# Optimization experiments

Hardware: AMD Instinct MI355X
Metric: run time of the kernel (lower is better)

Reference implementation:

```python
import jax, jax.numpy as jnp
import numpy as np

EPS = 1e-3  # keras BatchNormalization default epsilon
NUM_HEADS = 8


def conv1d_same(x, w, b):
    # x: [B,T,Cin], w: [K,Cin,Cout]
    return jax.lax.conv_general_dilated(
        x, w, window_strides=(1,), padding='SAME',
        dimension_numbers=('NWC', 'WIO', 'NWC')) + b


def bn(x, g, b, m, v):
    # inference-mode batchnorm with moving stats
    return (x - m) * jax.lax.rsqrt(v + EPS) * g + b


def lstm(x, K, R, b):
    # x: [B,T,D] -> [B,T,U]; keras gate order i,f,c,o; recurrent_dropout off at inference
    B = x.shape[0]
    U = R.shape[0]
    xp = jnp.einsum('btd,dz->btz', x, K) + b  # precompute input projection

    def step(carry, xt):
        h, c = carry
        z = xt + h @ R
        i, f, g, o = jnp.split(z, 4, axis=-1)
        c = jax.nn.sigmoid(f) * c + jax.nn.sigmoid(i) * jnp.tanh(g)
        h = jax.nn.sigmoid(o) * jnp.tanh(c)
        return (h, c), h

    h0 = jnp.zeros((B, U), x.dtype)
    _, hs = jax.lax.scan(step, (h0, h0), jnp.swapaxes(xp, 0, 1))
    return jnp.swapaxes(hs, 0, 1)


def bilstm(x, Kf, Rf, bf, Kb, Rb, bb):
    fwd = lstm(x, Kf, Rf, bf)
    bwd = lstm(x[:, ::-1], Kb, Rb, bb)[:, ::-1]
    return jnp.concatenate([fwd, bwd], axis=-1)


def mhsa(x, wq, bq, wk, bk, wv, bv, wo, bo):
    B, T, _ = x.shape
    d_model = wq.shape[1]
    dh = d_model // NUM_HEADS
    q = (x @ wq + bq).reshape(B, T, NUM_HEADS, dh)
    k = (x @ wk + bk).reshape(B, T, NUM_HEADS, dh)
    v = (x @ wv + bv).reshape(B, T, NUM_HEADS, dh)
    logits = jnp.einsum('bqhd,bkhd->bhqk', q, k) / jnp.sqrt(jnp.asarray(dh, x.dtype))
    attn = jax.nn.softmax(logits, axis=-1)
    out = jnp.einsum('bhqk,bkhd->bqhd', attn, v).reshape(B, T, d_model)
    return out @ wo + bo


def setup_inputs() -> dict:
    key = jax.random.key(0)
    ks = iter(jax.random.split(key, 64))

    def nrm(shape, s=0.05):
        return (jax.random.normal(next(ks), shape) * s).astype(jnp.float32)

    p = {}
    p['x'] = jax.random.normal(next(ks), (512, 256, 78), dtype=jnp.float32)
    for name, shp in [
            ('conv5_w', (5, 78, 64)), ('conv7_w', (7, 78, 64)), ('conv9_w', (9, 78, 64)),
            ('fuse_w', (1, 192, 128)), ('se_w1', (128, 8)), ('se_w2', (8, 128)),
            ('l1f_k', (128, 512)), ('l1f_r', (128, 512)), ('l1b_k', (128, 512)), ('l1b_r', (128, 512)),
            ('l2f_k', (256, 256)), ('l2f_r', (64, 256)), ('l2b_k', (256, 256)), ('l2b_r', (64, 256)),
            ('wq', (128, 256)), ('wk', (128, 256)), ('wv', (128, 256)), ('wo', (256, 256)),
            ('d1_w', (256, 256)), ('d2_w', (256, 128)), ('d3_w', (128, 1)),
            ('conv5_b', (64,)), ('conv7_b', (64,)), ('conv9_b', (64,)), ('fuse_b', (128,)),
            ('se_b1', (8,)), ('se_b2', (128,)),
            ('l1f_b', (512,)), ('l1b_b', (512,)), ('l2f_b', (256,)), ('l2b_b', (256,)),
            ('bq', (256,)), ('bk', (256,)), ('bv', (256,)), ('bo', (256,)),
            ('d1_b', (256,)), ('d2_b', (128,)), ('d3_b', (1,))]:
        p[name] = nrm(shp)
    for tag, c in [('bn5', 64), ('bn7', 64), ('bn9', 64), ('bn_l1', 256),
                   ('bn_l2', 128), ('bn_d1', 256), ('bn_d2', 128)]:
        p[tag + '_g'] = jnp.ones((c,), jnp.float32)
        p[tag + '_b'] = jnp.zeros((c,), jnp.float32)
        p[tag + '_m'] = jnp.zeros((c,), jnp.float32)
        p[tag + '_v'] = jnp.ones((c,), jnp.float32)
    return p


def reference(x, conv5_w, conv5_b, bn5_g, bn5_b, bn5_m, bn5_v,
              conv7_w, conv7_b, bn7_g, bn7_b, bn7_m, bn7_v,
              conv9_w, conv9_b, bn9_g, bn9_b, bn9_m, bn9_v,
              fuse_w, fuse_b, se_w1, se_b1, se_w2, se_b2,
              l1f_k, l1f_r, l1f_b, l1b_k, l1b_r, l1b_b,
              bn_l1_g, bn_l1_b, bn_l1_m, bn_l1_v,
              l2f_k, l2f_r, l2f_b, l2b_k, l2b_r, l2b_b,
              bn_l2_g, bn_l2_b, bn_l2_m, bn_l2_v,
              wq, bq, wk, bk, wv, bv, wo, bo,
              d1_w, d1_b, bn_d1_g, bn_d1_b, bn_d1_m, bn_d1_v,
              d2_w, d2_b, bn_d2_g, bn_d2_b, bn_d2_m, bn_d2_v,
              d3_w, d3_b):
    def block(w, b, g, bt, m, v):
        h = jax.nn.relu(conv1d_same(x, w, b))
        h = bn(h, g, bt, m, v)
        B, T, C = h.shape  # MaxPooling1D(2, 'same'); T is even
        return h.reshape(B, T // 2, 2, C).max(axis=2)

    fused = jnp.concatenate([
        block(conv5_w, conv5_b, bn5_g, bn5_b, bn5_m, bn5_v),
        block(conv7_w, conv7_b, bn7_g, bn7_b, bn7_m, bn7_v),
        block(conv9_w, conv9_b, bn9_g, bn9_b, bn9_m, bn9_v)], axis=-1)
    fused = conv1d_same(fused, fuse_w, fuse_b)

    # SENet spatial attention
    s = fused.mean(axis=1)
    e = jax.nn.sigmoid(jax.nn.relu(s @ se_w1 + se_b1) @ se_w2 + se_b2)
    h = fused * e[:, None, :]

    h = bilstm(h, l1f_k, l1f_r, l1f_b, l1b_k, l1b_r, l1b_b)
    h = bn(h, bn_l1_g, bn_l1_b, bn_l1_m, bn_l1_v)
    h = bilstm(h, l2f_k, l2f_r, l2f_b, l2b_k, l2b_r, l2b_b)
    h = bn(h, bn_l2_g, bn_l2_b, bn_l2_m, bn_l2_v)

    h = mhsa(h, wq, bq, wk, bk, wv, bv, wo, bo)
    g_ = h.mean(axis=1)

    d = jax.nn.relu(g_ @ d1_w + d1_b)
    d = bn(d, bn_d1_g, bn_d1_b, bn_d1_m, bn_d1_v)
    d = jax.nn.relu(d @ d2_w + d2_b)
    d = bn(d, bn_d2_g, bn_d2_b, bn_d2_m, bn_d2_v)
    return jax.nn.sigmoid(d @ d3_w + d3_b)
```

## Files before the change

### kernel.cpp

```cpp
#include <hip/hip_runtime.h>

#define EPS 1e-3f

typedef __attribute__((ext_vector_type(8))) short bf16x8;
typedef __attribute__((ext_vector_type(4))) float f32x4;

__device__ __forceinline__ float sigm(float x){ return 1.0f/(1.0f + __expf(-x)); }
__device__ __forceinline__ float tanhfast(float x){ return 1.0f - 2.0f/(1.0f + __expf(2.0f*x)); }

__device__ __forceinline__ unsigned short f2b(float f){
    union { float f; unsigned u; } v; v.f = f;
    unsigned r = v.u + 0x7FFFu + ((v.u >> 16) & 1u);
    return (unsigned short)(r >> 16);
}
__device__ __forceinline__ float b2f(unsigned short h){
    union { unsigned u; float f; } v; v.u = ((unsigned)h) << 16; return v.f;
}

__global__ void __launch_bounds__(256)
prep_x(const float* __restrict__ x, unsigned short* __restrict__ xbf)
{
    const int b = blockIdx.x;
    const float* xs = x + (size_t)b*256*78;
    unsigned short* xd = xbf + (size_t)b*264*96;
    for (int p = threadIdx.x; p < 264*48; p += 256){
        int row = p / 48;
        int cp  = (p - row*48) * 2;
        int t   = row - 4;
        unsigned short v0 = 0, v1 = 0;
        if (t >= 0 && t < 256){
            if (cp   < 78) v0 = f2b(xs[t*78 + cp]);
            if (cp+1 < 78) v1 = f2b(xs[t*78 + cp + 1]);
        }
        *(unsigned int*)(xd + row*96 + cp) = (unsigned)v0 | ((unsigned)v1 << 16);
    }
}

__global__ void __launch_bounds__(256)
prep_w(const float* __restrict__ w5, const float* __restrict__ w7, const float* __restrict__ w9,
       unsigned short* __restrict__ wfrag)
{
    int g = blockIdx.x*256 + threadIdx.x;
    if (g >= 27*12*64) return;
    union { unsigned short s[8]; uint4 v; } u;
    int base = g * 8;
    #pragma unroll
    for (int e = 0; e < 8; ++e){
        int lin  = base + e;
        int slot = lin & 511;
        int fi   = lin >> 9;
        int nt   = fi % 12, kcs = fi / 12;
        int k    = kcs / 3, cs = kcs - k*3;
        int l15  = slot >> 5, r = slot & 31;
        int lg   = r >> 3, ee = r & 7;
        int ci   = cs*32 + lg*8 + ee;
        int co   = nt*16 + l15;
        float val = 0.f;
        if (ci < 78){
            if (co < 64){
                int kk = k - 2;
                if (kk >= 0 && kk < 5) val = w5[(kk*78 + ci)*64 + co];
            } else if (co < 128){
                int kk = k - 1;
                if (kk >= 0 && kk < 7) val = w7[(kk*78 + ci)*64 + (co - 64)];
            } else {
                val = w9[(k*78 + ci)*64 + (co - 128)];
            }
        }
        u.s[e] = f2b(val);
    }
    *(uint4*)(wfrag + base) = u.v;
}

__global__ void prep_ss(const float* b5, const float* b7, const float* b9,
                        const float* g5, const float* be5, const float* m5, const float* v5,
                        const float* g7, const float* be7, const float* m7, const float* v7,
                        const float* g9, const float* be9, const float* m9, const float* v9,
                        float* __restrict__ biascat, float* __restrict__ scale, float* __restrict__ shift)
{
    int c = threadIdx.x;
    if (c >= 192) return;
    float bv, g, be, m, v;
    if (c < 64){        bv=b5[c];      g=g5[c];      be=be5[c];      m=m5[c];      v=v5[c]; }
    else if (c < 128){  int i=c-64;  bv=b7[i]; g=g7[i]; be=be7[i]; m=m7[i]; v=v7[i]; }
    else {              int i=c-128; bv=b9[i]; g=g9[i]; be=be9[i]; m=m9[i]; v=v9[i]; }
    float s = g * rsqrtf(v + EPS);
    biascat[c] = bv;
    scale[c]   = s;
    shift[c]   = be - m*s;
}

__global__ void __launch_bounds__(256)
conv_mfma(const unsigned short* __restrict__ xbf,
          const unsigned short* __restrict__ wfrag,
          const float* __restrict__ biascat, const float* __restrict__ scale,
          const float* __restrict__ shift,
          float* __restrict__ out)
{
    const int b = blockIdx.x, tile = blockIdx.y;
    const int tid = threadIdx.x, lane = tid & 63, wv = tid >> 6;
    const int l15 = lane & 15, lg = lane >> 4;
    const int nt0 = wv * 3;
    const int t0  = tile * 64;

    f32x4 acc[4][3];
    #pragma unroll
    for (int nt = 0; nt < 3; ++nt){
        float bv = biascat[(nt0 + nt)*16 + l15];
        #pragma unroll
        for (int mt = 0; mt < 4; ++mt)
            acc[mt][nt] = (f32x4){bv, bv, bv, bv};
    }

    const unsigned short* xb = xbf + ((size_t)b*264 + t0 + l15)*96 + lg*8;
    const unsigned short* wb = wfrag + (size_t)nt0*512 + l15*32 + lg*8;

    for (int k = 0; k < 9; ++k){
        #pragma unroll
        for (int cs = 0; cs < 3; ++cs){
            bf16x8 A[4], Bf[3];
            #pragma unroll
            for (int mt = 0; mt < 4; ++mt)
                A[mt] = *(const bf16x8*)(xb + (size_t)(k + mt*16)*96 + cs*32);
            #pragma unroll
            for (int nt = 0; nt < 3; ++nt)
                Bf[nt] = *(const bf16x8*)(wb + (size_t)((k*3 + cs)*12 + nt)*512);
            #pragma unroll
            for (int mt = 0; mt < 4; ++mt)
                #pragma unroll
                for (int nt = 0; nt < 3; ++nt)
                    acc[mt][nt] = __builtin_amdgcn_mfma_f32_16x16x32_bf16(A[mt], Bf[nt], acc[mt][nt], 0, 0, 0);
        }
    }

    #pragma unroll
    for (int nt = 0; nt < 3; ++nt){
        int col = (nt0 + nt)*16 + l15;
        float s = scale[col], sh = shift[col];
        #pragma unroll
        for (int mt = 0; mt < 4; ++mt){
            float v0 = fmaxf(acc[mt][nt][0], 0.f)*s + sh;
            float v1 = fmaxf(acc[mt][nt][1], 0.f)*s + sh;
            float v2 = fmaxf(acc[mt][nt][2], 0.f)*s + sh;
            float v3 = fmaxf(acc[mt][nt][3], 0.f)*s + sh;
            int tb = tile*32 + mt*8 + lg*2;
            out[((size_t)b*128 + tb    )*192 + col] = fmaxf(v0, v1);
            out[((size_t)b*128 + tb + 1)*192 + col] = fmaxf(v2, v3);
        }
    }
}

__global__ void __launch_bounds__(256)
fuse_v2(const float* __restrict__ in,
        const float* __restrict__ w,
        const float* __restrict__ bias,
        float* __restrict__ out)
{
    __shared__ float xl[16][192];
    const int tid = threadIdx.x;
    const size_t row0 = (size_t)blockIdx.x * 16;

    {
        const float4* ip = (const float4*)(in + row0*192);
        float4* xp = (float4*)&xl[0][0];
        #pragma unroll
        for (int idx = tid; idx < 768; idx += 256) xp[idx] = ip[idx];
    }
    __syncthreads();

    const int co = tid & 127;
    const int rg = tid >> 7;
    float acc[8];
    {
        float bv = bias[co];
        #pragma unroll
        for (int r = 0; r < 8; ++r) acc[r] = bv;
    }

    for (int ci4 = 0; ci4 < 192; ci4 += 4){
        float wv0 = w[(ci4+0)*128 + co];
        float wv1 = w[(ci4+1)*128 + co];
        float wv2 = w[(ci4+2)*128 + co];
        float wv3 = w[(ci4+3)*128 + co];
        #pragma unroll
        for (int r = 0; r < 8; ++r){
            const float4 xr = *(const float4*)&xl[rg*8 + r][ci4];
            acc[r] = fmaf(xr.x, wv0, acc[r]);
            acc[r] = fmaf(xr.y, wv1, acc[r]);
            acc[r] = fmaf(xr.z, wv2, acc[r]);
            acc[r] = fmaf(xr.w, wv3, acc[r]);
        }
    }
    #pragma unroll
    for (int r = 0; r < 8; ++r)
        out[(row0 + rg*8 + r)*128 + co] = acc[r];
}

__global__ void se_kernel(float* __restrict__ fused,
                          const float* __restrict__ w1, const float* __restrict__ b1,
                          const float* __restrict__ w2, const float* __restrict__ b2)
{
    int b = blockIdx.x, c = threadIdx.x;
    __shared__ float sv[128];
    __shared__ float rv[8];
    float* fp = fused + (size_t)b*128*128 + c;
    float acc = 0.f;
    for (int t = 0; t < 128; ++t) acc += fp[t*128];
    sv[c] = acc * (1.f/128.f);
    __syncthreads();
    if (c < 8){
        float r = b1[c];
        for (int i = 0; i < 128; ++i) r = fmaf(sv[i], w1[i*8 + c], r);
        rv[c] = fmaxf(r, 0.f);
    }
    __syncthreads();
    float e = b2[c];
    #pragma unroll
    for (int j = 0; j < 8; ++j) e = fmaf(rv[j], w2[j*128 + c], e);
    e = sigm(e);
    for (int t = 0; t < 128; ++t) fp[t*128] *= e;
}

template<int K, bool ABF16, int OUTMODE>
__global__ void __launch_bounds__(256)
xp_gemm(const void* __restrict__ Av, const float* __restrict__ W,
        const float* __restrict__ bias, unsigned short* __restrict__ outp, int N)
{
    __shared__ unsigned short Asm[128][40];
    __shared__ unsigned short Bsm[8][64][8];

    const int tid  = threadIdx.x;
    const int lane = tid & 63;
    const int wv   = tid >> 6;
    const int wm   = wv & 1;
    const int wn   = wv >> 1;
    const size_t m0 = (size_t)blockIdx.x * 128;
    const int n0   = blockIdx.y * 128;

    f32x4 acc[4][4];
    #pragma unroll
    for (int nt = 0; nt < 4; ++nt){
        float bv = bias[n0 + wn*64 + nt*16 + (lane & 15)];
        #pragma unroll
        for (int mt = 0; mt < 4; ++mt)
            acc[mt][nt] = (f32x4){bv, bv, bv, bv};
    }

    const int bn = tid & 127;
    const int bg = tid >> 7;

    for (int k0 = 0; k0 < K; k0 += 32){
        __syncthreads();
        if constexpr (!ABF16){
            const float* Ag = (const float*)Av;
            #pragma unroll
            for (int i = 0; i < 2; ++i){
                int g = tid + i*256;
                int r = g >> 2, c8 = g & 3;
                float4 d0 = *(const float4*)(Ag + (m0 + r)*K + k0 + c8*8);
                float4 d1 = *(const float4*)(Ag + (m0 + r)*K + k0 + c8*8 + 4);
                union { unsigned short s[8]; uint4 v; } u;
                u.s[0]=f2b(d0.x); u.s[1]=f2b(d0.y); u.s[2]=f2b(d0.z); u.s[3]=f2b(d0.w);
                u.s[4]=f2b(d1.x); u.s[5]=f2b(d1.y); u.s[6]=f2b(d1.z); u.s[7]=f2b(d1.w);
                *(uint4*)&Asm[r][c8*8] = u.v;
            }
        } else {
            const unsigned short* Ag = (const unsigned short*)Av;
            #pragma unroll
            for (int i = 0; i < 2; ++i){
                int g = tid + i*256;
                int r = g >> 2, c8 = g & 3;
                uint4 d = *(const uint4*)(Ag + (m0 + r)*K + k0 + c8*8);
                *(uint4*)&Asm[r][c8*8] = d;
            }
        }
        {
            union { unsigned short s[8]; uint4 v; } u0, u1;
            #pragma unroll
            for (int q = 0; q < 8; ++q){
                u0.s[q] = f2b(W[(size_t)(k0 + bg*16 + q)*N + n0 + bn]);
                u1.s[q] = f2b(W[(size_t)(k0 + bg*16 + 8 + q)*N + n0 + bn]);
            }
            int nt = bn >> 4, lo = bn & 15;
            *(uint4*)&Bsm[nt][lo + 16*(2*bg)][0]   = u0.v;
            *(uint4*)&Bsm[nt][lo + 16*(2*bg+1)][0] = u1.v;
        }
        __syncthreads();

        bf16x8 af[4], bfr[4];
        #pragma unroll
        for (int mt = 0; mt < 4; ++mt)
            af[mt] = *(const bf16x8*)&Asm[wm*64 + mt*16 + (lane & 15)][(lane >> 4)*8];
        #pragma unroll
        for (int nt = 0; nt < 4; ++nt)
            bfr[nt] = *(const bf16x8*)&Bsm[wn*4 + nt][lane][0];
        #pragma unroll
        for (int mt = 0; mt < 4; ++mt)
            #pragma unroll
            for (int nt = 0; nt < 4; ++nt)
                acc[mt][nt] = __builtin_amdgcn_mfma_f32_16x16x32_bf16(af[mt], bfr[nt], acc[mt][nt], 0, 0, 0);
    }

    #pragma unroll
    for (int mt = 0; mt < 4; ++mt)
        #pragma unroll
        for (int nt = 0; nt < 4; ++nt)
            #pragma unroll
            for (int r = 0; r < 4; ++r){
                size_t row = m0 + wm*64 + mt*16 + (lane >> 4)*4 + r;
                int    col = n0 + wn*64 + nt*16 + (lane & 15);
                if constexpr (OUTMODE == 0){
                    outp[row*N + col] = f2b(acc[mt][nt][r]);
                } else {
                    size_t off = ((size_t)((row >> 7)*8 + (col >> 5))*32 + (col & 31))*128 + (row & 127);
                    outp[off] = f2b(acc[mt][nt][r]);
                }
            }
}

template<int U, bool OUT_BF16>
__global__ void __launch_bounds__(512)
lstm_rec(const unsigned short* __restrict__ xpf, const unsigned short* __restrict__ xpb,
         const float* __restrict__ Rf, const float* __restrict__ Rb,
         const float* __restrict__ bng, const float* __restrict__ bnb,
         const float* __restrict__ bnm, const float* __restrict__ bnv,
         void* __restrict__ outv, int dir_param)
{
    constexpr int Z   = 4*U;
    constexpr int KT  = U/32;
    constexpr int NTW = Z/128;
    constexpr int HP  = U + 8;

    __shared__ unsigned short h_lds[16][HP];
    __shared__ float z_lds[4][Z];

    const int tid  = threadIdx.x;
    const int lane = tid & 63;
    const int wv   = tid >> 6;
    const int dir  = (gridDim.y == 2) ? (int)blockIdx.y : dir_param;
    const int b0   = blockIdx.x * 4;
    const int ncol0 = wv * (Z/8);

    const unsigned short* xp = dir ? xpb : xpf;
    const float* Rg = dir ? Rb : Rf;

    for (int i = tid; i < 16*HP; i += 512) ((unsigned short*)h_lds)[i] = 0;

    bf16x8 rf[KT][NTW];
    {
        const int kb = (lane >> 4) * 8;
        const int nc = lane & 15;
        #pragma unroll
        for (int kt = 0; kt < KT; ++kt)
            #pragma unroll
            for (int nt = 0; nt < NTW; ++nt){
                union { unsigned short s[8]; bf16x8 v; } u;
                #pragma unroll
                for (int e = 0; e < 8; ++e)
                    u.s[e] = f2b(Rg[(size_t)(kt*32 + kb + e)*Z + ncol0 + nt*16 + nc]);
                rf[kt][nt] = u.v;
            }
    }

    const int u_  = tid % U;
    const int r_  = tid / U;
    const bool gate = (tid < 4*U);
    float c_ = 0.f;
    float bns = 0.f, bnsh = 0.f;
    const int ch = dir*U + u_;
    if (gate){
        bns  = bng[ch] * rsqrtf(bnv[ch] + EPS);
        bnsh = bnb[ch] - bnm[ch]*bns;
    }
    __syncthreads();

    for (int ts = 0; ts < 128; ++ts){
        const int t = dir ? 127 - ts : ts;
        unsigned short xq0=0,xq1=0,xq2=0,xq3=0;
        if (gate){
            const unsigned short* xr = xp + ((size_t)(b0 + r_)*128 + t)*Z + u_;
            xq0 = xr[0]; xq1 = xr[U]; xq2 = xr[2*U]; xq3 = xr[3*U];
        }
        bf16x8 af[KT];
        #pragma unroll
        for (int kt = 0; kt < KT; ++kt)
            af[kt] = *(const bf16x8*)&h_lds[lane & 15][kt*32 + (lane >> 4)*8];
        f32x4 acc[NTW];
        #pragma unroll
        for (int nt = 0; nt < NTW; ++nt) acc[nt] = (f32x4){0.f,0.f,0.f,0.f};
        #pragma unroll
        for (int kt = 0; kt < KT; ++kt)
            #pragma unroll
            for (int nt = 0; nt < NTW; ++nt)
                acc[nt] = __builtin_amdgcn_mfma_f32_16x16x32_bf16(af[kt], rf[kt][nt], acc[nt], 0, 0, 0);
        if ((lane >> 4) == 0){
            #pragma unroll
            for (int nt = 0; nt < NTW; ++nt)
                #pragma unroll
                for (int r = 0; r < 4; ++r)
                    z_lds[r][ncol0 + nt*16 + (lane & 15)] = acc[nt][r];
        }
        __syncthreads();
        if (gate){
            float z0 = z_lds[r_][u_      ] + b2f(xq0);
            float z1 = z_lds[r_][u_ +  U ] + b2f(xq1);
            float z2 = z_lds[r_][u_ + 2*U] + b2f(xq2);
            float z3 = z_lds[r_][u_ + 3*U] + b2f(xq3);
            float iv = sigm(z0), fv = sigm(z1), gv = tanhfast(z2), ov = sigm(z3);
            c_ = fv*c_ + iv*gv;
            float h = ov * tanhfast(c_);
            h_lds[r_][u_] = f2b(h);
            float hb = fmaf(h, bns, bnsh);
            size_t oidx = ((size_t)(b0 + r_)*128 + t)*(size_t)(2*U) + ch;
            if constexpr (OUT_BF16) ((unsigned short*)outv)[oidx] = f2b(hb);
            else                    ((float*)outv)[oidx] = hb;
        }
        __syncthreads();
    }
}

__global__ void __launch_bounds__(256)
attn_kernel(const unsigned short* __restrict__ qb,
            const unsigned short* __restrict__ kb,
            const unsigned short* __restrict__ vb,
            float* __restrict__ msum)
{
    __shared__ unsigned short p_lds[128][136];
    __shared__ float red[4][2][16];

    const int b  = blockIdx.x, hd = blockIdx.y;
    const int tid = threadIdx.x, lane = tid & 63, wv = tid >> 6;
    const int m0 = wv * 32;
    const int l15 = lane & 15, lg = lane >> 4;

    bf16x8 aq[2];
    #pragma unroll
    for (int mt = 0; mt < 2; ++mt)
        aq[mt] = *(const bf16x8*)(qb + ((size_t)(b*128 + m0 + mt*16 + l15))*256 + hd*32 + lg*8);

    bf16x8 bk[8];
    #pragma unroll
    for (int nt = 0; nt < 8; ++nt)
        bk[nt] = *(const bf16x8*)(kb + ((size_t)(b*128 + nt*16 + l15))*256 + hd*32 + lg*8);

    f32x4 s[2][8];
    #pragma unroll
    for (int mt = 0; mt < 2; ++mt)
        #pragma unroll
        for (int nt = 0; nt < 8; ++nt) s[mt][nt] = (f32x4){0.f,0.f,0.f,0.f};
    #pragma unroll
    for (int mt = 0; mt < 2; ++mt)
        #pragma unroll
        for (int nt = 0; nt < 8; ++nt)
            s[mt][nt] = __builtin_amdgcn_mfma_f32_16x16x32_bf16(aq[mt], bk[nt], s[mt][nt], 0, 0, 0);

    const float scale = 0.17677669529663687f;
    #pragma unroll
    for (int mt = 0; mt < 2; ++mt)
        #pragma unroll
        for (int r = 0; r < 4; ++r){
            float mx = -1e30f;
            #pragma unroll
            for (int nt = 0; nt < 8; ++nt) mx = fmaxf(mx, s[mt][nt][r]);
            #pragma unroll
            for (int msk = 1; msk < 16; msk <<= 1) mx = fmaxf(mx, __shfl_xor(mx, msk, 64));
            float pv[8], sum = 0.f;
            #pragma unroll
            for (int nt = 0; nt < 8; ++nt){
                pv[nt] = __expf((s[mt][nt][r] - mx) * scale);
                sum += pv[nt];
            }
            #pragma unroll
            for (int msk = 1; msk < 16; msk <<= 1) sum += __shfl_xor(sum, msk, 64);
            float inv = 1.f / sum;
            int row = m0 + mt*16 + lg*4 + r;
            #pragma unroll
            for (int nt = 0; nt < 8; ++nt)
                p_lds[row][nt*16 + l15] = f2b(pv[nt] * inv);
        }
    __syncthreads();

    f32x4 o[2][2];
    #pragma unroll
    for (int mt = 0; mt < 2; ++mt)
        #pragma unroll
        for (int dn = 0; dn < 2; ++dn) o[mt][dn] = (f32x4){0.f,0.f,0.f,0.f};
    bf16x8 bv[4][2];
    #pragma unroll
    for (int kt = 0; kt < 4; ++kt)
        #pragma unroll
        for (int dn = 0; dn < 2; ++dn)
            bv[kt][dn] = *(const bf16x8*)(vb + ((size_t)(b*8 + hd)*32 + dn*16 + l15)*128 + kt*32 + lg*8);
    #pragma unroll
    for (int mt = 0; mt < 2; ++mt)
        #pragma unroll
        for (int kt = 0; kt < 4; ++kt){
            bf16x8 ap = *(const bf16x8*)&p_lds[m0 + mt*16 + l15][kt*32 + lg*8];
            #pragma unroll
            for (int dn = 0; dn < 2; ++dn)
                o[mt][dn] = __builtin_amdgcn_mfma_f32_16x16x32_bf16(ap, bv[kt][dn], o[mt][dn], 0, 0, 0);
        }

    float sm[2];
    #pragma unroll
    for (int dn = 0; dn < 2; ++dn){
        float a = 0.f;
        #pragma unroll
        for (int mt = 0; mt < 2; ++mt)
            #pragma unroll
            for (int r = 0; r < 4; ++r) a += o[mt][dn][r];
        a += __shfl_xor(a, 16, 64);
        a += __shfl_xor(a, 32, 64);
        sm[dn] = a;
    }
    if (lg == 0){
        red[wv][0][l15] = sm[0];
        red[wv][1][l15] = sm[1];
    }
    __syncthreads();
    if (tid < 32){
        int dn = tid >> 4, n = tid & 15;
        float tot = red[0][dn][n] + red[1][dn][n] + red[2][dn][n] + red[3][dn][n];
        msum[(size_t)b*256 + hd*32 + dn*16 + n] = tot * (1.f/128.f);
    }
}

__global__ void __launch_bounds__(256)
head_kernel(const float* __restrict__ msum,
            const float* __restrict__ wo, const float* __restrict__ bo,
            const float* __restrict__ d1w, const float* __restrict__ d1b,
            const float* __restrict__ g1, const float* __restrict__ b1,
            const float* __restrict__ m1, const float* __restrict__ v1,
            const float* __restrict__ d2w, const float* __restrict__ d2b,
            const float* __restrict__ g2, const float* __restrict__ b2,
            const float* __restrict__ m2, const float* __restrict__ v2,
            const float* __restrict__ d3w, const float* __restrict__ d3b,
            float* __restrict__ outp)
{
    int b = blockIdx.x, j = threadIdx.x;
    __shared__ float s1[256];
    __shared__ float s2[256];
    const float* mr = msum + (size_t)b*256;
    float acc = bo[j];
    #pragma unroll 4
    for (int i = 0; i < 256; ++i) acc = fmaf(mr[i], wo[i*256 + j], acc);
    s1[j] = acc;
    __syncthreads();
    float a1 = d1b[j];
    #pragma unroll 4
    for (int i = 0; i < 256; ++i) a1 = fmaf(s1[i], d1w[i*256 + j], a1);
    a1 = fmaxf(a1, 0.f);
    float sc1 = g1[j] * rsqrtf(v1[j] + EPS);
    a1 = a1 * sc1 + (b1[j] - m1[j] * sc1);
    s2[j] = a1;
    __syncthreads();
    if (j < 128){
        float a2 = d2b[j];
        #pragma unroll 4
        for (int i = 0; i < 256; ++i) a2 = fmaf(s2[i], d2w[i*128 + j], a2);
        a2 = fmaxf(a2, 0.f);
        float sc2 = g2[j] * rsqrtf(v2[j] + EPS);
        a2 = a2 * sc2 + (b2[j] - m2[j] * sc2);
        s1[j] = a2;
    }
    __syncthreads();
    if (j == 0){
        float a3 = d3b[0];
        for (int i = 0; i < 128; ++i) a3 = fmaf(s1[i], d3w[i], a3);
        outp[b] = sigm(a3);
    }
}

extern "C" void kernel_launch(void* const* d_in, const int* in_sizes, int n_in,
                              void* d_out, int out_size, void* d_ws, size_t ws_size,
                              hipStream_t stream)
{
    #define F(i) ((const float*)d_in[i])
    const float* x       = F(0);
    const float* conv5_w = F(1);
    const float* conv7_w = F(2);
    const float* conv9_w = F(3);
    const float* fuse_w  = F(4);
    const float* se_w1   = F(5);
    const float* se_w2   = F(6);
    const float* l1f_k   = F(7);
    const float* l1f_r   = F(8);
    const float* l1b_k   = F(9);
    const float* l1b_r   = F(10);
    const float* l2f_k   = F(11);
    const float* l2f_r   = F(12);
    const float* l2b_k   = F(13);
    const float* l2b_r   = F(14);
    const float* wq      = F(15);
    const float* wk      = F(16);
    const float* wv      = F(17);
    const float* wo      = F(18);
    const float* d1_w    = F(19);
    const float* d2_w    = F(20);
    const float* d3_w    = F(21);
    const float* conv5_b = F(22);
    const float* conv7_b = F(23);
    const float* conv9_b = F(24);
    const float* fuse_b  = F(25);
    const float* se_b1   = F(26);
    const float* se_b2   = F(27);
    const float* l1f_b   = F(28);
    const float* l1b_b   = F(29);
    const float* l2f_b   = F(30);
    const float* l2b_b   = F(31);
    const float* bq      = F(32);
    const float* bk      = F(33);
    const float* bv      = F(34);
    const float* bo      = F(35);
    const float* d1_b    = F(36);
    const float* d2_b    = F(37);
    const float* d3_b    = F(38);
    const float* bn5_g = F(39), *bn5_b = F(40), *bn5_m = F(41), *bn5_v = F(42);
    const float* bn7_g = F(43), *bn7_b = F(44), *bn7_m = F(45), *bn7_v = F(46);
    const float* bn9_g = F(47), *bn9_b = F(48), *bn9_m = F(49), *bn9_v = F(50);
    const float* bnl1_g = F(51), *bnl1_b = F(52), *bnl1_m = F(53), *bnl1_v = F(54);
    const float* bnl2_g = F(55), *bnl2_b = F(56), *bnl2_m = F(57), *bnl2_v = F(58);
    const float* bnd1_g = F(59), *bnd1_b = F(60), *bnd1_m = F(61), *bnd1_v = F(62);
    const float* bnd2_g = F(63), *bnd2_b = F(64), *bnd2_m = F(65), *bnd2_v = F(66);
    #undef F

    float* ws = (float*)d_ws;
    float* concat = ws;
    float* fused  = ws + 12582912;
    unsigned short* xbf   = (unsigned short*)(ws + 20971520);
    unsigned short* wfrag = (unsigned short*)(ws + 27607040);
    float* biascat = ws + 27689984;
    float* cscale  = ws + 27690176;
    float* cshift  = ws + 27690368;
    unsigned short* xp1f  = (unsigned short*)(ws);
    unsigned short* xp1b  = (unsigned short*)(ws + 20971520);
    unsigned short* l1out = (unsigned short*)(ws + 29360128);
    unsigned short* xp2f  = (unsigned short*)(ws);
    unsigned short* xp2b  = (unsigned short*)(ws + 4194304);
    unsigned short* l2out = (unsigned short*)(ws + 8388608);
    unsigned short* qbuf  = (unsigned short*)(ws + 12582912);
    unsigned short* kbuf  = (unsigned short*)(ws);
    unsigned short* vbuf  = (unsigned short*)(ws + 20971520);
    float* msum   = ws + 29360128;
    float* outp   = (float*)d_out;

    prep_x<<<dim3(512), dim3(256), 0, stream>>>(x, xbf);
    prep_w<<<dim3(81), dim3(256), 0, stream>>>(conv5_w, conv7_w, conv9_w, wfrag);
    prep_ss<<<dim3(1), dim3(192), 0, stream>>>(
        conv5_b, conv7_b, conv9_b,
        bn5_g, bn5_b, bn5_m, bn5_v,
        bn7_g, bn7_b, bn7_m, bn7_v,
        bn9_g, bn9_b, bn9_m, bn9_v,
        biascat, cscale, cshift);
    conv_mfma<<<dim3(512,4), dim3(256), 0, stream>>>(
        xbf, wfrag, biascat, cscale, cshift, concat);

    fuse_v2<<<dim3(4096), dim3(256), 0, stream>>>(concat, fuse_w, fuse_b, fused);
    se_kernel<<<dim3(512), dim3(128), 0, stream>>>(fused, se_w1, se_b1, se_w2, se_b2);

    xp_gemm<128,false,0><<<dim3(512,4), dim3(256), 0, stream>>>(fused, l1f_k, l1f_b, xp1f, 512);
    xp_gemm<128,false,0><<<dim3(512,4), dim3(256), 0, stream>>>(fused, l1b_k, l1b_b, xp1b, 512);
    lstm_rec<128,true><<<dim3(128,2), dim3(512), 0, stream>>>(
        xp1f, xp1b, l1f_r, l1b_r, bnl1_g, bnl1_b, bnl1_m, bnl1_v, l1out, 0);

    xp_gemm<256,true,0><<<dim3(512,2), dim3(256), 0, stream>>>(l1out, l2f_k, l2f_b, xp2f, 256);
    xp_gemm<256,true,0><<<dim3(512,2), dim3(256), 0, stream>>>(l1out, l2b_k, l2b_b, xp2b, 256);
    lstm_rec<64,true><<<dim3(128,2), dim3(512), 0, stream>>>(
        xp2f, xp2b, l2f_r, l2b_r, bnl2_g, bnl2_b, bnl2_m, bnl2_v, l2out, 0);

    xp_gemm<128,true,0><<<dim3(512,2), dim3(256), 0, stream>>>(l2out, wq, bq, qbuf, 256);
    xp_gemm<128,true,0><<<dim3(512,2), dim3(256), 0, stream>>>(l2out, wk, bk, kbuf, 256);
    xp_gemm<128,true,1><<<dim3(512,2), dim3(256), 0, stream>>>(l2out, wv, bv, vbuf, 256);

    attn_kernel<<<dim3(512,8), dim3(256), 0, stream>>>(qbuf, kbuf, vbuf, msum);

    head_kernel<<<dim3(512), dim3(256), 0, stream>>>(
        msum, wo, bo,
        d1_w, d1_b, bnd1_g, bnd1_b, bnd1_m, bnd1_v,
        d2_w, d2_b, bnd2_g, bnd2_b, bnd2_m, bnd2_v,
        d3_w, d3_b, outp);

    (void)in_sizes; (void)n_in; (void)out_size; (void)ws_size;
}
```

Before: 716.3 us.

## Fold SE scaling into LSTM input GEMM, use MFMA for fuse conv, halve LSTM batch per block

Replaces the scalar fp32 1x1 fuse conv with the bf16 MFMA GEMM kernel, which writes bf16 output. The SE kernel now only computes per-batch channel scales, and those scales are applied while loading the A tile of the layer-1 input projection, removing a read-modify-write pass. The LSTM input projections are written gate-interleaved so each step loads one ushort4, and that load is prefetched one timestep ahead. Recurrent blocks now handle 2 batch rows instead of 4, doubling block count for more parallelism. Storing the fused activations in bf16 adds rounding before the SE mean.

```diff
diff --git a/kernel.cpp b/kernel.cpp
--- a/kernel.cpp
+++ b/kernel.cpp
@@ -150,62 +150,18 @@
     }
 }
 
-__global__ void __launch_bounds__(256)
-fuse_v2(const float* __restrict__ in,
-        const float* __restrict__ w,
-        const float* __restrict__ bias,
-        float* __restrict__ out)
-{
-    __shared__ float xl[16][192];
-    const int tid = threadIdx.x;
-    const size_t row0 = (size_t)blockIdx.x * 16;
-
-    {
-        const float4* ip = (const float4*)(in + row0*192);
-        float4* xp = (float4*)&xl[0][0];
-        #pragma unroll
-        for (int idx = tid; idx < 768; idx += 256) xp[idx] = ip[idx];
-    }
-    __syncthreads();
-
-    const int co = tid & 127;
-    const int rg = tid >> 7;
-    float acc[8];
-    {
-        float bv = bias[co];
-        #pragma unroll
-        for (int r = 0; r < 8; ++r) acc[r] = bv;
-    }
-
-    for (int ci4 = 0; ci4 < 192; ci4 += 4){
-        float wv0 = w[(ci4+0)*128 + co];
-        float wv1 = w[(ci4+1)*128 + co];
-        float wv2 = w[(ci4+2)*128 + co];
-        float wv3 = w[(ci4+3)*128 + co];
-        #pragma unroll
-        for (int r = 0; r < 8; ++r){
-            const float4 xr = *(const float4*)&xl[rg*8 + r][ci4];
-            acc[r] = fmaf(xr.x, wv0, acc[r]);
-            acc[r] = fmaf(xr.y, wv1, acc[r]);
-            acc[r] = fmaf(xr.z, wv2, acc[r]);
-            acc[r] = fmaf(xr.w, wv3, acc[r]);
-        }
-    }
-    #pragma unroll
-    for (int r = 0; r < 8; ++r)
-        out[(row0 + rg*8 + r)*128 + co] = acc[r];
-}
-
-__global__ void se_kernel(float* __restrict__ fused,
-                          const float* __restrict__ w1, const float* __restrict__ b1,
-                          const float* __restrict__ w2, const float* __restrict__ b2)
+__global__ void __launch_bounds__(128)
+se_mean(const unsigned short* __restrict__ fb,
+        const float* __restrict__ w1, const float* __restrict__ b1,
+        const float* __restrict__ w2, const float* __restrict__ b2,
+        float* __restrict__ e)
 {
     int b = blockIdx.x, c = threadIdx.x;
     __shared__ float sv[128];
     __shared__ float rv[8];
-    float* fp = fused + (size_t)b*128*128 + c;
+    const unsigned short* fp = fb + (size_t)b*128*128 + c;
     float acc = 0.f;
-    for (int t = 0; t < 128; ++t) acc += fp[t*128];
+    for (int t = 0; t < 128; ++t) acc += b2f(fp[t*128]);
     sv[c] = acc * (1.f/128.f);
     __syncthreads();
     if (c < 8){
@@ -214,20 +170,21 @@
         rv[c] = fmaxf(r, 0.f);
     }
     __syncthreads();
-    float e = b2[c];
-    #pragma unroll
-    for (int j = 0; j < 8; ++j) e = fmaf(rv[j], w2[j*128 + c], e);
-    e = sigm(e);
-    for (int t = 0; t < 128; ++t) fp[t*128] *= e;
-}
-
-template<int K, bool ABF16, int OUTMODE>
+    float ev = b2[c];
+    #pragma unroll
+    for (int j = 0; j < 8; ++j) ev = fmaf(rv[j], w2[j*128 + c], ev);
+    e[(size_t)b*128 + c] = sigm(ev);
+}
+
+template<int K, bool ABF16, int OUTMODE, bool ESCALE>
 __global__ void __launch_bounds__(256)
 xp_gemm(const void* __restrict__ Av, const float* __restrict__ W,
-        const float* __restrict__ bias, unsigned short* __restrict__ outp, int N)
+        const float* __restrict__ bias, const float* __restrict__ esc,
+        unsigned short* __restrict__ outp, int N)
 {
     __shared__ unsigned short Asm[128][40];
     __shared__ unsigned short Bsm[8][64][8];
+    __shared__ float esm[ESCALE ? K : 1];
 
     const int tid  = threadIdx.x;
     const int lane = tid & 63;
@@ -236,6 +193,10 @@
     const int wn   = wv >> 1;
     const size_t m0 = (size_t)blockIdx.x * 128;
     const int n0   = blockIdx.y * 128;
+
+    if constexpr (ESCALE){
+        for (int i = tid; i < K; i += 256) esm[i] = esc[(size_t)blockIdx.x*K + i];
+    }
 
     f32x4 acc[4][4];
     #pragma unroll
@@ -271,6 +232,12 @@
                 int g = tid + i*256;
                 int r = g >> 2, c8 = g & 3;
                 uint4 d = *(const uint4*)(Ag + (m0 + r)*K + k0 + c8*8);
+                if constexpr (ESCALE){
+                    unsigned short* s = (unsigned short*)&d;
+                    #pragma unroll
+                    for (int j = 0; j < 8; ++j)
+                        s[j] = f2b(b2f(s[j]) * esm[k0 + c8*8 + j]);
+                }
                 *(uint4*)&Asm[r][c8*8] = d;
             }
         }
@@ -311,20 +278,23 @@
                 int    col = n0 + wn*64 + nt*16 + (lane & 15);
                 if constexpr (OUTMODE == 0){
                     outp[row*N + col] = f2b(acc[mt][nt][r]);
-                } else {
+                } else if constexpr (OUTMODE == 1){
                     size_t off = ((size_t)((row >> 7)*8 + (col >> 5))*32 + (col & 31))*128 + (row & 127);
                     outp[off] = f2b(acc[mt][nt][r]);
+                } else {
+                    const int U = N/4;
+                    outp[row*N + (col & (U-1))*4 + (col / U)] = f2b(acc[mt][nt][r]);
                 }
             }
 }
 
-template<int U, bool OUT_BF16>
+template<int U, int RB, bool OUT_BF16>
 __global__ void __launch_bounds__(512)
 lstm_rec(const unsigned short* __restrict__ xpf, const unsigned short* __restrict__ xpb,
          const float* __restrict__ Rf, const float* __restrict__ Rb,
          const float* __restrict__ bng, const float* __restrict__ bnb,
          const float* __restrict__ bnm, const float* __restrict__ bnv,
-         void* __restrict__ outv, int dir_param)
+         void* __restrict__ outv)
 {
     constexpr int Z   = 4*U;
     constexpr int KT  = U/32;
@@ -337,8 +307,8 @@
     const int tid  = threadIdx.x;
     const int lane = tid & 63;
     const int wv   = tid >> 6;
-    const int dir  = (gridDim.y == 2) ? (int)blockIdx.y : dir_param;
-    const int b0   = blockIdx.x * 4;
+    const int dir  = blockIdx.y;
+    const int b0   = blockIdx.x * RB;
     const int ncol0 = wv * (Z/8);
 
     const unsigned short* xp = dir ? xpb : xpf;
@@ -364,7 +334,7 @@
 
     const int u_  = tid % U;
     const int r_  = tid / U;
-    const bool gate = (tid < 4*U);
+    const bool gate = (tid < RB*U);
     float c_ = 0.f;
     float bns = 0.f, bnsh = 0.f;
     const int ch = dir*U + u_;
@@ -372,14 +342,18 @@
         bns  = bng[ch] * rsqrtf(bnv[ch] + EPS);
         bnsh = bnb[ch] - bnm[ch]*bns;
     }
-    __syncthreads();
+    const unsigned short* xbase = xp + (size_t)(b0 + (gate ? r_ : 0))*128*Z + u_*4;
+    __syncthreads();
+
+    ushort4 xq = {0,0,0,0};
+    if (gate) xq = *(const ushort4*)(xbase + (size_t)(dir ? 127 : 0)*Z);
 
     for (int ts = 0; ts < 128; ++ts){
         const int t = dir ? 127 - ts : ts;
-        unsigned short xq0=0,xq1=0,xq2=0,xq3=0;
-        if (gate){
-            const unsigned short* xr = xp + ((size_t)(b0 + r_)*128 + t)*Z + u_;
-            xq0 = xr[0]; xq1 = xr[U]; xq2 = xr[2*U]; xq3 = xr[3*U];
+        ushort4 xn = xq;
+        if (gate && ts < 127){
+            int tn = dir ? t - 1 : t + 1;
+            xn = *(const ushort4*)(xbase + (size_t)tn*Z);
         }
         bf16x8 af[KT];
         #pragma unroll
@@ -402,10 +376,10 @@
         }
         __syncthreads();
         if (gate){
-            float z0 = z_lds[r_][u_      ] + b2f(xq0);
-            float z1 = z_lds[r_][u_ +  U ] + b2f(xq1);
-            float z2 = z_lds[r_][u_ + 2*U] + b2f(xq2);
-            float z3 = z_lds[r_][u_ + 3*U] + b2f(xq3);
+            float z0 = z_lds[r_][u_      ] + b2f(xq.x);
+            float z1 = z_lds[r_][u_ +  U ] + b2f(xq.y);
+            float z2 = z_lds[r_][u_ + 2*U] + b2f(xq.z);
+            float z3 = z_lds[r_][u_ + 3*U] + b2f(xq.w);
             float iv = sigm(z0), fv = sigm(z1), gv = tanhfast(z2), ov = sigm(z3);
             c_ = fv*c_ + iv*gv;
             float h = ov * tanhfast(c_);
@@ -416,6 +390,7 @@
             else                    ((float*)outv)[oidx] = hb;
         }
         __syncthreads();
+        xq = xn;
     }
 }
 
@@ -626,7 +601,8 @@
 
     float* ws = (float*)d_ws;
     float* concat = ws;
-    float* fused  = ws + 12582912;
+    unsigned short* fusedbf = (unsigned short*)(ws + 12582912);
+    float* e      = ws + 16777216;
     unsigned short* xbf   = (unsigned short*)(ws + 20971520);
     unsigned short* wfrag = (unsigned short*)(ws + 27607040);
     float* biascat = ws + 27689984;
@@ -655,22 +631,30 @@
     conv_mfma<<<dim3(512,4), dim3(256), 0, stream>>>(
         xbf, wfrag, biascat, cscale, cshift, concat);
 
-    fuse_v2<<<dim3(4096), dim3(256), 0, stream>>>(concat, fuse_w, fuse_b, fused);
-    se_kernel<<<dim3(512), dim3(128), 0, stream>>>(fused, se_w1, se_b1, se_w2, se_b2);
-
-    xp_gemm<128,false,0><<<dim3(512,4), dim3(256), 0, stream>>>(fused, l1f_k, l1f_b, xp1f, 512);
-    xp_gemm<128,false,0><<<dim3(512,4), dim3(256), 0, stream>>>(fused, l1b_k, l1b_b, xp1b, 512);
-    lstm_rec<128,true><<<dim3(128,2), dim3(512), 0, stream>>>(
-        xp1f, xp1b, l1f_r, l1b_r, bnl1_g, bnl1_b, bnl1_m, bnl1_v, l1out, 0);
-
-    xp_gemm<256,true,0><<<dim3(512,2), dim3(256), 0, stream>>>(l1out, l2f_k, l2f_b, xp2f, 256);
-    xp_gemm<256,true,0><<<dim3(512,2), dim3(256), 0, stream>>>(l1out, l2b_k, l2b_b, xp2b, 256);
-    lstm_rec<64,true><<<dim3(128,2), dim3(512), 0, stream>>>(
-        xp2f, xp2b, l2f_r, l2b_r, bnl2_g, bnl2_b, bnl2_m, bnl2_v, l2out, 0);
-
-    xp_gemm<128,true,0><<<dim3(512,2), dim3(256), 0, stream>>>(l2out, wq, bq, qbuf, 256);
-    xp_gemm<128,true,0><<<dim3(512,2), dim3(256), 0, stream>>>(l2out, wk, bk, kbuf, 256);
-    xp_gemm<128,true,1><<<dim3(512,2), dim3(256), 0, stream>>>(l2out, wv, bv, vbuf, 256);
+    xp_gemm<192,false,0,false><<<dim3(512,1), dim3(256), 0, stream>>>(
+        concat, fuse_w, fuse_b, nullptr, fusedbf, 128);
+    se_mean<<<dim3(512), dim3(128), 0, stream>>>(fusedbf, se_w1, se_b1, se_w2, se_b2, e);
+
+    xp_gemm<128,true,2,true><<<dim3(512,4), dim3(256), 0, stream>>>(
+        fusedbf, l1f_k, l1f_b, e, xp1f, 512);
+    xp_gemm<128,true,2,true><<<dim3(512,4), dim3(256), 0, stream>>>(
+        fusedbf, l1b_k, l1b_b, e, xp1b, 512);
+    lstm_rec<128,2,true><<<dim3(256,2), dim3(512), 0, stream>>>(
+        xp1f, xp1b, l1f_r, l1b_r, bnl1_g, bnl1_b, bnl1_m, bnl1_v, l1out);
+
+    xp_gemm<256,true,2,false><<<dim3(512,2), dim3(256), 0, stream>>>(
+        l1out, l2f_k, l2f_b, nullptr, xp2f, 256);
+    xp_gemm<256,true,2,false><<<dim3(512,2), dim3(256), 0, stream>>>(
+        l1out, l2b_k, l2b_b, nullptr, xp2b, 256);
+    lstm_rec<64,2,true><<<dim3(256,2), dim3(512), 0, stream>>>(
+        xp2f, xp2b, l2f_r, l2b_r, bnl2_g, bnl2_b, bnl2_m, bnl2_v, l2out);
+
+    xp_gemm<128,true,0,false><<<dim3(512,2), dim3(256), 0, stream>>>(
+        l2out, wq, bq, nullptr, qbuf, 256);
+    xp_gemm<128,true,0,false><<<dim3(512,2), dim3(256), 0, stream>>>(
+        l2out, wk, bk, nullptr, kbuf, 256);
+    xp_gemm<128,true,1,false><<<dim3(512,2), dim3(256), 0, stream>>>(
+        l2out, wv, bv, nullptr, vbuf, 256);
 
     attn_kernel<<<dim3(512,8), dim3(256), 0, stream>>>(qbuf, kbuf, vbuf, msum);
 
```

Result: slower. 775.8 us (+8.3%).
